# Performance work log

Hardware: AMD Instinct MI355X
Metric: run time of the kernel (lower is better)

The kernel has to match this reference:

```python
import jax, jax.numpy as jnp
import numpy as np

jax.config.update("jax_enable_x64", True)

B, N, M_EQ, D_INEQ = 64, 128, 32, 64
RHO = 1.0
THRES = 1e-5
MAX_ITERS = 5000  # safety cap (original loops until relative objective change <= 1e-5)


def setup_inputs() -> dict:
    key = jax.random.key(0)
    kL, kq, kG, kA, kx0, ks = jax.random.split(key, 6)
    L = jax.random.normal(kL, (B, N, N))
    Q = jnp.einsum('bij,bkj->bik', L, L) / N + jnp.eye(N)  # SPD, well-conditioned
    q = jax.random.normal(kq, (B, N))
    G = jax.random.normal(kG, (B, D_INEQ, N))
    A = jax.random.normal(kA, (B, M_EQ, N))
    x0 = jax.random.normal(kx0, (B, N))
    slack = jax.random.uniform(ks, (B, D_INEQ)) + 0.1
    h = jnp.einsum('bdn,bn->bd', G, x0) + slack  # strictly feasible ineq
    b = jnp.einsum('bmn,bn->bm', A, x0)          # feasible eq
    f32 = jnp.float32
    return {"Q": Q.astype(f32), "q": q.astype(f32), "G": G.astype(f32),
            "h": h.astype(f32), "A": A.astype(f32), "b": b.astype(f32)}


def _alt_diff_batch(Q, q, G, h, A, b):
    """Batched Alt-Diff ADMM QP solve; returns (x [B,n], dx/dq [B,n,n])."""
    Bb, n = q.shape
    d = h.shape[1]
    m = b.shape[1]
    dt = Q.dtype
    AtA = jnp.einsum('bmi,bmj->bij', A, A)
    GtG = jnp.einsum('bdi,bdj->bij', G, G)
    R = -jnp.linalg.inv(Q + RHO * AtA + RHO * GtG)
    ATb = RHO * jnp.einsum('bmn,bm->bn', A, b)
    GTh = RHO * jnp.einsum('bdn,bd->bn', G, h)
    eye = jnp.eye(n, dtype=dt)

    def obj(x):
        return 0.5 * jnp.einsum('bi,bij,bj->b', x, Q, x) + jnp.einsum('bi,bi->b', q, x)

    init = dict(
        xk=jnp.zeros((Bb, n), dt), sk=jnp.zeros((Bb, d), dt),
        lamb=jnp.zeros((Bb, m), dt), nu=jnp.zeros((Bb, d), dt),
        dxk=jnp.zeros((Bb, n, n), dt), dsk=jnp.zeros((Bb, d, n), dt),
        dlamb=jnp.zeros((Bb, m, n), dt), dnu=jnp.zeros((Bb, d, n), dt),
        res_prev=jnp.full((Bb,), 1000.0, dt),   # res = [1000, -100] init
        res_cur=jnp.full((Bb,), -100.0, dt),
        done=jnp.zeros((Bb,), bool),
        it=jnp.zeros((), jnp.int32),
    )

    def cond(s):
        return jnp.logical_and(jnp.any(~s["done"]), s["it"] < MAX_ITERS)

    def body(s):
        xk = jnp.einsum('bij,bj->bi', R,
                        q + jnp.einsum('bmn,bm->bn', A, s["lamb"])
                          + jnp.einsum('bdn,bd->bn', G, s["nu"]) - ATb
                          + RHO * jnp.einsum('bdn,bd->bn', G, s["sk"]) - GTh)
        dxk = jnp.einsum('bij,bjk->bik', R,
                         eye + jnp.einsum('bmn,bmk->bnk', A, s["dlamb"])
                             + jnp.einsum('bdn,bdk->bnk', G, s["dnu"])
                             + RHO * jnp.einsum('bdn,bdk->bnk', G, s["dsk"]))
        Gx = jnp.einsum('bdn,bn->bd', G, xk)
        sk = jax.nn.relu(-(1.0 / RHO) * s["nu"] - (Gx - h))
        sgn = (sk > 0).astype(dt)  # sgn applied to already-relu'd sk, as in source
        dsk = (-1.0 / RHO) * sgn[:, :, None] * (s["dnu"] + RHO * jnp.einsum('bdn,bnk->bdk', G, dxk))
        lamb = s["lamb"] + RHO * (jnp.einsum('bmn,bn->bm', A, xk) - b)
        dlamb = s["dlamb"] + RHO * jnp.einsum('bmn,bnk->bmk', A, dxk)
        nu = s["nu"] + RHO * (Gx + sk - h)
        dnu = s["dnu"] + RHO * (jnp.einsum('bdn,bnk->bdk', G, dxk) + dsk)
        res_new = obj(xk)

        keep = s["done"]

        def sel(old, new):
            mask = keep.reshape((-1,) + (1,) * (new.ndim - 1))
            return jnp.where(mask, old, new)

        res_prev = jnp.where(keep, s["res_prev"], s["res_cur"])
        res_cur = jnp.where(keep, s["res_cur"], res_new)
        done = keep | (jnp.abs((res_cur - res_prev) / res_prev) <= THRES)
        return dict(
            xk=sel(s["xk"], xk), sk=sel(s["sk"], sk),
            lamb=sel(s["lamb"], lamb), nu=sel(s["nu"], nu),
            dxk=sel(s["dxk"], dxk), dsk=sel(s["dsk"], dsk),
            dlamb=sel(s["dlamb"], dlamb), dnu=sel(s["dnu"], dnu),
            res_prev=res_prev, res_cur=res_cur, done=done, it=s["it"] + 1,
        )

    final = jax.lax.while_loop(cond, body, init)
    return final["xk"], final["dxk"]


def reference(Q, q, G, h, A, b):
    out_dtype = q.dtype
    f64 = jnp.float64
    x, _dx = _alt_diff_batch(Q.astype(f64), q.astype(f64), G.astype(f64),
                             h.astype(f64), A.astype(f64), b.astype(f64))
    return x.astype(out_dtype)
```

## Files before the change

### kernel.cpp

```cpp
#include <hip/hip_runtime.h>

#define NN 128
#define ME 32
#define DI 64
#define NZ 96
#define ROWD 130
#define MAXIT 5000

#define OFF_UN 16640
#define ROWB  (OFF_UN)
#define COLB  (OFF_UN + 256)
#define PLO2  (OFF_UN)
#define PHI2  (OFF_UN + 512)
#define TV0   (OFF_UN + 768)
#define TV1   (OFF_UN + 896)
#define FLG   (OFF_UN + 928)
#define YBUF  (OFF_UN)
#define KBUF  (OFF_UN + 1536)
#define CPART (OFF_UN + 1024)
#define VP    (OFF_UN + 1280)
#define BASEV (OFF_UN + 1792)
#define QBV   (OFF_UN + 1888)
#define FPART (OFF_UN + 1024)
#define RHSV  (OFF_UN + 1280)
#define XPART (OFF_UN + 1408)
#define CB    (OFF_UN + 2688)
#define QBUF  (OFF_UN + 2816)
#define V1    (OFF_UN + 2944)
#define V2    (OFF_UN + 3072)
#define HB    (OFF_UN + 3200)
#define BB    (OFF_UN + 3264)
#define CST   (OFF_UN + 3296)
#define ZBF   (OFF_UN + 3304)
#define LDS_DBL (OFF_UN + 3400)

__device__ __forceinline__ float rlf(float v, int lane) {
  return __uint_as_float((unsigned)__builtin_amdgcn_readlane((int)__float_as_uint(v), lane));
}

__global__ __launch_bounds__(256, 1) void altdiff_kernel(
    const float* __restrict__ Qg, const float* __restrict__ qg,
    const float* __restrict__ Gg, const float* __restrict__ hg,
    const float* __restrict__ Ag, const float* __restrict__ bg,
    float* __restrict__ out)
{
  extern __shared__ double ldsd[];
  double2* lds2 = (double2*)ldsd;

  const int bidx = blockIdx.x;
  const int tid  = threadIdx.x;
  const int w    = tid >> 6;
  const int l    = tid & 63;
  const int lm   = l & 31;
  const int ia   = tid & 127;
  const int hh   = tid >> 7;

  const float* Qb = Qg + (size_t)bidx * NN * NN;
  const float* Ab = Ag + (size_t)bidx * ME * NN;
  const float* Gb = Gg + (size_t)bidx * DI * NN;
  const float* qb = qg + (size_t)bidx * NN;
  const float* hb = hg + (size_t)bidx * DI;
  const float* bv = bg + (size_t)bidx * ME;

  if (tid < DI) ldsd[HB + tid] = (double)hb[tid];
  else if (tid < DI + ME) ldsd[BB + tid - DI] = (double)bv[tid - DI];
  if (tid >= 128) ldsd[QBUF + tid - 128] = (double)qb[tid - 128];

  const int r = tid >> 4, c = tid & 15;
  double acc[8][8];

  {
    const float4* Q4 = (const float4*)Qb;
#pragma unroll
    for (int rr = 0; rr < 8; ++rr) {
      float4 q0 = Q4[((8*r+rr) << 5) + 2*c];
      float4 q1 = Q4[((8*r+rr) << 5) + 2*c + 1];
      acc[rr][0]=(double)q0.x; acc[rr][1]=(double)q0.y; acc[rr][2]=(double)q0.z; acc[rr][3]=(double)q0.w;
      acc[rr][4]=(double)q1.x; acc[rr][5]=(double)q1.y; acc[rr][6]=(double)q1.z; acc[rr][7]=(double)q1.w;
    }
    const float4* A4 = (const float4*)Ab;
    for (int m = 0; m < ME; ++m) {
      float4 u0 = A4[(m << 5) + 2*r], u1 = A4[(m << 5) + 2*r + 1];
      float4 v0 = A4[(m << 5) + 2*c], v1 = A4[(m << 5) + 2*c + 1];
      double uu[8] = {(double)u0.x,(double)u0.y,(double)u0.z,(double)u0.w,
                      (double)u1.x,(double)u1.y,(double)u1.z,(double)u1.w};
      double vv[8] = {(double)v0.x,(double)v0.y,(double)v0.z,(double)v0.w,
                      (double)v1.x,(double)v1.y,(double)v1.z,(double)v1.w};
#pragma unroll
      for (int rr = 0; rr < 8; ++rr)
#pragma unroll
        for (int cc = 0; cc < 8; ++cc)
          acc[rr][cc] = fma(uu[rr], vv[cc], acc[rr][cc]);
    }
    const float4* G4 = (const float4*)Gb;
    for (int d = 0; d < DI; ++d) {
      float4 u0 = G4[(d << 5) + 2*r], u1 = G4[(d << 5) + 2*r + 1];
      float4 v0 = G4[(d << 5) + 2*c], v1 = G4[(d << 5) + 2*c + 1];
      double uu[8] = {(double)u0.x,(double)u0.y,(double)u0.z,(double)u0.w,
                      (double)u1.x,(double)u1.y,(double)u1.z,(double)u1.w};
      double vv[8] = {(double)v0.x,(double)v0.y,(double)v0.z,(double)v0.w,
                      (double)v1.x,(double)v1.y,(double)v1.z,(double)v1.w};
#pragma unroll
      for (int rr = 0; rr < 8; ++rr)
#pragma unroll
        for (int cc = 0; cc < 8; ++cc)
          acc[rr][cc] = fma(uu[rr], vv[cc], acc[rr][cc]);
    }
  }

  {
    if (r == 0) {
#pragma unroll
      for (int cc = 0; cc < 8; ++cc) ldsd[ROWB + 8*c + cc] = acc[0][cc];
    }
    if (c == 0) {
#pragma unroll
      for (int rr = 0; rr < 8; ++rr) ldsd[COLB + 8*r + rr] = acc[rr][0];
    }
    __syncthreads();
    for (int k = 0; k < NN; ++k) {
      const int pb = (k & 1) << 7;
      const int krt = k >> 3, kcl = k & 7;
      double rowk[8], colv[8];
#pragma unroll
      for (int cc = 0; cc < 8; ++cc) rowk[cc] = ldsd[ROWB + pb + 8*c + cc];
#pragma unroll
      for (int rr = 0; rr < 8; ++rr) colv[rr] = ldsd[COLB + pb + 8*r + rr];
      const double dkk  = ldsd[ROWB + pb + k];
      const double rcpd = 1.0 / dkk;
      double rdv[8];
#pragma unroll
      for (int cc = 0; cc < 8; ++cc) rdv[cc] = rowk[cc] * rcpd;
      const bool pivR = (r == krt), pivC = (c == krt);
#pragma unroll
      for (int rr = 0; rr < 8; ++rr) {
        const double cv = colv[rr] * rcpd;
        const bool pr = pivR && (rr == kcl);
#pragma unroll
        for (int cc = 0; cc < 8; ++cc) {
          double gen = fma(-cv, rowk[cc], acc[rr][cc]);
          acc[rr][cc] = pr ? rdv[cc] : gen;
        }
      }
      if (pivC) {
#pragma unroll
        for (int cc = 0; cc < 8; ++cc) if (cc == kcl) {
#pragma unroll
          for (int rr = 0; rr < 8; ++rr) {
            const bool pr2 = pivR && (rr == kcl);
            acc[rr][cc] = pr2 ? -rcpd : colv[rr] * rcpd;
          }
        }
      }
      if (k < NN - 1) {
        const int pb2 = ((k + 1) & 1) << 7;
        const int krt2 = (k + 1) >> 3, kcl2 = (k + 1) & 7;
        if (r == krt2) {
#pragma unroll
          for (int rr = 0; rr < 8; ++rr) if (rr == kcl2) {
#pragma unroll
            for (int cc = 0; cc < 8; ++cc) ldsd[ROWB + pb2 + 8*c + cc] = acc[rr][cc];
          }
        }
        if (c == krt2) {
#pragma unroll
          for (int cc = 0; cc < 8; ++cc) if (cc == kcl2) {
#pragma unroll
            for (int rr = 0; rr < 8; ++rr) ldsd[COLB + pb2 + 8*r + rr] = acc[rr][cc];
          }
        }
      }
      __syncthreads();
    }
#pragma unroll
    for (int rr = 0; rr < 8; ++rr) {
      double2* dst = (double2*)(ldsd + (8*r+rr)*ROWD + 8*c);
#pragma unroll
      for (int t = 0; t < 4; ++t) dst[t] = make_double2(acc[rr][2*t], acc[rr][2*t+1]);
    }
  }
  __syncthreads();

  float Kf[24], Kf2[24];
  for (int blk = 0; blk < 8; ++blk) {
    {
      const float* gp[6];
#pragma unroll
      for (int jj = 0; jj < 6; ++jj) {
        int it = 12*blk + 6*hh + jj;
        gp[jj] = (it < DI) ? (Gb + it*NN) : (Ab + (it - DI)*NN);
      }
      double a2[6] = {0,0,0,0,0,0};
#pragma unroll 4
      for (int t = 0; t < NN; ++t) {
        double rv = ldsd[t*ROWD + ia];
#pragma unroll
        for (int jj = 0; jj < 6; ++jj)
          a2[jj] = fma(rv, (double)gp[jj][t], a2[jj]);
      }
      double2* yst = (double2*)(ldsd + YBUF + ia*12 + 6*hh);
#pragma unroll
      for (int p = 0; p < 3; ++p) yst[p] = make_double2(a2[2*p], a2[2*p+1]);
    }
    __syncthreads();
    {
      const int r2 = (ia < NZ) ? ia : 0;
      const float* brow = (r2 < DI) ? (Gb + r2*NN) : (Ab + (r2 - DI)*NN);
      double a2[6] = {0,0,0,0,0,0};
#pragma unroll 4
      for (int t = 0; t < NN; ++t) {
        double bvv = (double)brow[t];
        const double2* yr = (const double2*)(ldsd + YBUF + t*12 + 6*hh);
        double2 y0 = yr[0], y1 = yr[1], y2 = yr[2];
        a2[0] = fma(bvv, y0.x, a2[0]); a2[1] = fma(bvv, y0.y, a2[1]);
        a2[2] = fma(bvv, y1.x, a2[2]); a2[3] = fma(bvv, y1.y, a2[3]);
        a2[4] = fma(bvv, y2.x, a2[4]); a2[5] = fma(bvv, y2.y, a2[5]);
      }
      if (ia < NZ) {
#pragma unroll
        for (int jj = 0; jj < 6; ++jj) ldsd[KBUF + (6*hh + jj)*NZ + ia] = a2[jj];
      }
    }
    __syncthreads();
    if (w == (blk >> 1)) {
      if ((blk & 1) == 0) {
#pragma unroll
        for (int jj = 0; jj < 12; ++jj) {
          Kf [jj] = (float)ldsd[KBUF + jj*NZ + l];
          Kf2[jj] = (float)ldsd[KBUF + jj*NZ + 64 + lm];
        }
      } else {
#pragma unroll
        for (int jj = 0; jj < 12; ++jj) {
          Kf [12+jj] = (float)ldsd[KBUF + jj*NZ + l];
          Kf2[12+jj] = (float)ldsd[KBUF + jj*NZ + 64 + lm];
        }
      }
    }
    __syncthreads();
  }

  {
    double s = 0;
#pragma unroll 8
    for (int jc = 0; jc < 48; ++jc) {
      int j = 48*hh + jc;
      double coef = (j < DI) ? ldsd[HB + j] : ldsd[BB + j - DI];
      const float* src = (j < DI) ? (Gb + j*NN) : (Ab + (j - DI)*NN);
      s = fma(-(double)src[ia], coef, s);
    }
    ldsd[CPART + hh*128 + ia] = s;
  }
  __syncthreads();
  if (tid < NN) ldsd[CB + tid] = ldsd[QBUF + tid] + ldsd[CPART + tid] + ldsd[CPART + 128 + tid];
  __syncthreads();

  {
    double a = 0, b2 = 0;
#pragma unroll 4
    for (int tt = 0; tt < 64; ++tt) {
      int t = 64*hh + tt;
      double rv = ldsd[t*ROWD + ia];
      a  = fma(rv, ldsd[CB + t], a);
      b2 = fma(rv, ldsd[QBUF + t], b2);
    }
    ldsd[VP + hh*128 + ia] = a;
    ldsd[VP + 256 + hh*128 + ia] = b2;
  }
  __syncthreads();
  if (tid < NN) {
    ldsd[V1 + tid] = ldsd[VP + tid] + ldsd[VP + 128 + tid];
    ldsd[V2 + tid] = ldsd[VP + 256 + tid] + ldsd[VP + 384 + tid];
  }
  __syncthreads();

  {
    const int r2 = (ia < NZ) ? ia : 0;
    const float* brow = (r2 < DI) ? (Gb + r2*NN) : (Ab + (r2 - DI)*NN);
    const int voff = hh ? V2 : V1;
    double s = 0;
#pragma unroll 4
    for (int t = 0; t < NN; ++t) s = fma((double)brow[t], ldsd[voff + t], s);
    if (ia < NZ) ldsd[(hh ? QBV : BASEV) + ia] = s;
  }
  if (w == 0) {
    double pc = ldsd[V1+l]*ldsd[CB+l]   + ldsd[V1+64+l]*ldsd[CB+64+l];
    double pq = ldsd[V1+l]*ldsd[QBUF+l] + ldsd[V1+64+l]*ldsd[QBUF+64+l];
#pragma unroll
    for (int off = 32; off >= 1; off >>= 1) { pc += __shfl_xor(pc, off); pq += __shfl_xor(pq, off); }
    if (l == 0) { ldsd[CST] = pc; ldsd[CST+1] = pq; }
  }
  __syncthreads();

  const double h_r   = ldsd[HB + l];
  const double b_r   = ldsd[BB + lm];
  const double baseA = ldsd[BASEV + l];
  const double baseB = ldsd[BASEV + 64 + lm];
  const double qvA   = ldsd[QBV + l];
  const double qvB   = ldsd[QBV + 64 + lm];
  const double S_uc  = ldsd[CST], S_qu = ldsd[CST + 1];
  double nu = 0.0, lam = 0.0;
  double zlo = 0.0, zhi = 0.0;
  double zAlo = 0.0, zAhi = 0.0, zBlo = 0.0, zBhi = 0.0, zClo = 0.0, zChi = 0.0;
  double res_prev = 1000.0, res_cur = -100.0;

  {
    double a0 = (w == 0) ? baseA : 0.0;
    double a1 = (w == 0) ? baseB : 0.0;
    ldsd[PLO2 + w*64 + l] = a0;
    if (l < 32) ldsd[PHI2 + w*32 + l] = a1;
    if (tid == 0) { ldsd[FLG] = 0.0; ldsd[FLG + 1] = 0.0; }
  }

  for (int it = 0; it < MAXIT + 3; ++it) {
    __syncthreads();
    const int p  = (it & 1) << 8;
    const int ph = (it & 1) << 7;
    const int bprev = (it + 1) & 1;
    double fl = ldsd[FLG + bprev];
    double t1v[16];
    if (w == 1) {
      const double2* tp = (const double2*)(ldsd + TV1 + bprev*16);
#pragma unroll
      for (int u = 0; u < 8; ++u) { double2 v = tp[u]; t1v[2*u] = v.x; t1v[2*u+1] = v.y; }
    }
    double a40 = 0, a41 = 0, a42 = 0, a43 = 0;
    if (w == 3) {
      const double2* t0p = (const double2*)(ldsd + TV0 + bprev*64 + (l & 15)*4);
      double2 v0 = t0p[0], v1 = t0p[1];
      a40 = v0.x; a41 = v0.y; a42 = v1.x; a43 = v1.y;
    }
    double ylo = 0.0, yhi = 0.0;
    if (w != 3)
      ylo = (ldsd[PLO2 + p + l]       + ldsd[PLO2 + p + 64 + l])
          + (ldsd[PLO2 + p + 128 + l] + ldsd[PLO2 + p + 192 + l]);
    if (w >= 2)
      yhi = (ldsd[PHI2 + ph + lm]      + ldsd[PHI2 + ph + 32 + lm])
          + (ldsd[PHI2 + ph + 64 + lm] + ldsd[PHI2 + ph + 96 + lm]);
    if (it >= 3 && fl != 0.0) break;
    if (w == 2) { zClo = zBlo; zChi = zBhi; zBlo = zAlo; zBhi = zAhi; zAlo = zlo; zAhi = zhi; }
    if (it < MAXIT) {
      if (w != 3) {
        double sk = fmax(0.0, -nu - ylo + h_r);
        nu  = nu + ylo + sk - h_r;
        zlo = nu + sk;
      }
      if (w >= 2) {
        lam = lam + yhi - b_r;
        zhi = lam;
      }
      const float zflo = (float)zlo;
      const float zfhi = (float)zhi;
      float a0f = 0.f, a0g = 0.f, a1f = 0.f, a1g = 0.f;
      if (w == 0) {
#pragma unroll
        for (int j = 0; j < 24; j += 2) {
          float zj  = rlf(zflo, j);
          float zj1 = rlf(zflo, j + 1);
          a0f = fmaf(Kf[j],   zj,  a0f); a1f = fmaf(Kf2[j],   zj,  a1f);
          a0g = fmaf(Kf[j+1], zj1, a0g); a1g = fmaf(Kf2[j+1], zj1, a1g);
        }
      } else if (w == 1) {
#pragma unroll
        for (int j = 0; j < 24; j += 2) {
          float zj  = rlf(zflo, 24 + j);
          float zj1 = rlf(zflo, 24 + j + 1);
          a0f = fmaf(Kf[j],   zj,  a0f); a1f = fmaf(Kf2[j],   zj,  a1f);
          a0g = fmaf(Kf[j+1], zj1, a0g); a1g = fmaf(Kf2[j+1], zj1, a1g);
        }
      } else if (w == 2) {
#pragma unroll
        for (int j = 0; j < 16; j += 2) {
          float zj  = rlf(zflo, 48 + j);
          float zj1 = rlf(zflo, 48 + j + 1);
          a0f = fmaf(Kf[j],   zj,  a0f); a1f = fmaf(Kf2[j],   zj,  a1f);
          a0g = fmaf(Kf[j+1], zj1, a0g); a1g = fmaf(Kf2[j+1], zj1, a1g);
        }
#pragma unroll
        for (int j = 0; j < 8; j += 2) {
          float zj  = rlf(zfhi, j);
          float zj1 = rlf(zfhi, j + 1);
          a0f = fmaf(Kf[16+j],   zj,  a0f); a1f = fmaf(Kf2[16+j],   zj,  a1f);
          a0g = fmaf(Kf[16+j+1], zj1, a0g); a1g = fmaf(Kf2[16+j+1], zj1, a1g);
        }
      } else {
#pragma unroll
        for (int j = 0; j < 24; j += 2) {
          float zj  = rlf(zfhi, 8 + j);
          float zj1 = rlf(zfhi, 8 + j + 1);
          a0f = fmaf(Kf[j],   zj,  a0f); a1f = fmaf(Kf2[j],   zj,  a1f);
          a0g = fmaf(Kf[j+1], zj1, a0g); a1g = fmaf(Kf2[j+1], zj1, a1g);
        }
      }
      double pa0 = (double)(a0f + a0g);
      double pa1 = (double)(a1f + a1g);
      if (w == 0) { pa0 += baseA; pa1 += baseB; }
      ldsd[PLO2 + (p ^ 256) + w*64 + l] = pa0;
      if (l < 32) ldsd[PHI2 + (ph ^ 128) + w*32 + l] = pa1;
      if (w == 2) {
        double tv = fma(qvA, zAlo, -0.5*(zAlo*(baseA + ylo) + ylo*ylo));
        tv += (l < 32) ? fma(qvB, zAhi, -0.5*(zAhi*(baseB + yhi) + yhi*yhi)) : 0.0;
        ldsd[TV0 + (it & 1)*64 + l] = tv;
      }
    }
    if (w == 3 && l < 16 && it >= 1 && it <= MAXIT)
      ldsd[TV1 + (it & 1)*16 + l] = (a40 + a41) + (a42 + a43);
    if (w == 1 && it >= 2 && it <= MAXIT + 1) {
      double s1 = ((t1v[0] + t1v[1]) + (t1v[2] + t1v[3])) + ((t1v[4] + t1v[5]) + (t1v[6] + t1v[7]));
      double s2 = ((t1v[8] + t1v[9]) + (t1v[10] + t1v[11])) + ((t1v[12] + t1v[13]) + (t1v[14] + t1v[15]));
      double obj = (s1 + s2) - 0.5*S_uc + S_qu;
      res_prev = res_cur; res_cur = obj;
      if (l == 0)
        ldsd[FLG + (it & 1)] = (fabs((res_cur - res_prev) / res_prev) <= 1e-5) ? 1.0 : 0.0;
    }
  }

  if (w == 2) {
    ldsd[ZBF + l] = zClo;
    if (l < 32) ldsd[ZBF + 64 + l] = zChi;
  }
  __syncthreads();
  {
    double s = 0;
#pragma unroll 8
    for (int jc = 0; jc < 48; ++jc) {
      int j = 48*hh + jc;
      double zj = ldsd[ZBF + j];
      const float* src = (j < DI) ? (Gb + j*NN) : (Ab + (j - DI)*NN);
      s = fma((double)src[ia], zj, s);
    }
    ldsd[FPART + hh*128 + ia] = s;
  }
  __syncthreads();
  if (tid < NN) ldsd[RHSV + tid] = ldsd[CB + tid] + ldsd[FPART + tid] + ldsd[FPART + 128 + tid];
  __syncthreads();
  {
    double s = 0;
#pragma unroll 4
    for (int tt = 0; tt < 64; ++tt) {
      int t = 64*hh + tt;
      s = fma(ldsd[t*ROWD + ia], ldsd[RHSV + t], s);
    }
    ldsd[XPART + hh*128 + ia] = s;
  }
  __syncthreads();
  if (tid < NN)
    out[(size_t)bidx * NN + tid] = (float)(ldsd[XPART + tid] + ldsd[XPART + 128 + tid]);
}

extern "C" void kernel_launch(void* const* d_in, const int* in_sizes, int n_in,
                              void* d_out, int out_size, void* d_ws, size_t ws_size,
                              hipStream_t stream) {
  (void)in_sizes; (void)n_in; (void)out_size; (void)d_ws; (void)ws_size;
  const float* Q = (const float*)d_in[0];
  const float* q = (const float*)d_in[1];
  const float* G = (const float*)d_in[2];
  const float* h = (const float*)d_in[3];
  const float* A = (const float*)d_in[4];
  const float* b = (const float*)d_in[5];
  float* out = (float*)d_out;
  const size_t lds_bytes = (size_t)LDS_DBL * sizeof(double);
  altdiff_kernel<<<dim3(64), dim3(256), lds_bytes, stream>>>(Q, q, G, h, A, b, out);
}
```

Baseline: 656.5 us.

## Pack per-wave partial sums as interleaved floats and use packed FMA in ADMM loop

The per-iteration partial products across the four waves are now stored as fp32, interleaved four per element with an XOR swizzle, so each lane reads them back with one float4 load instead of four separate double loads. The matvec uses two-wide float vectors so the compiler can emit packed FMA instructions. The baseA/baseB addition moves to the reader, the nu/sk update is simplified algebraically, and the convergence test replaces the division with a multiply. Partial sums are now stored and reduced in float rather than double, which slightly changes the rounding of y.

```diff
diff --git a/kernel.cpp b/kernel.cpp
--- a/kernel.cpp
+++ b/kernel.cpp
@@ -10,11 +10,11 @@
 #define OFF_UN 16640
 #define ROWB  (OFF_UN)
 #define COLB  (OFF_UN + 256)
-#define PLO2  (OFF_UN)
-#define PHI2  (OFF_UN + 512)
-#define TV0   (OFF_UN + 768)
-#define TV1   (OFF_UN + 896)
-#define FLG   (OFF_UN + 928)
+#define FPLO  (2*OFF_UN)
+#define FPHI  (2*OFF_UN + 512)
+#define TV0   (OFF_UN + 384)
+#define TV1   (OFF_UN + 512)
+#define FLG   (OFF_UN + 544)
 #define YBUF  (OFF_UN)
 #define KBUF  (OFF_UN + 1536)
 #define CPART (OFF_UN + 1024)
@@ -34,8 +34,13 @@
 #define ZBF   (OFF_UN + 3304)
 #define LDS_DBL (OFF_UN + 3400)
 
+typedef __attribute__((ext_vector_type(2))) float f32x2;
+
 __device__ __forceinline__ float rlf(float v, int lane) {
   return __uint_as_float((unsigned)__builtin_amdgcn_readlane((int)__float_as_uint(v), lane));
+}
+__device__ __forceinline__ f32x2 fma2(f32x2 a, f32x2 b, f32x2 c) {
+  return __builtin_elementwise_fma(a, b, c);
 }
 
 __global__ __launch_bounds__(256, 1) void altdiff_kernel(
@@ -45,7 +50,7 @@
     float* __restrict__ out)
 {
   extern __shared__ double ldsd[];
-  double2* lds2 = (double2*)ldsd;
+  float* const ldsf = (float*)ldsd;
 
   const int bidx = blockIdx.x;
   const int tid  = threadIdx.x;
@@ -181,7 +186,7 @@
   }
   __syncthreads();
 
-  float Kf[24], Kf2[24];
+  f32x2 Kp[12], Kp2[12];
   for (int blk = 0; blk < 8; ++blk) {
     {
       const float* gp[6];
@@ -225,15 +230,19 @@
     if (w == (blk >> 1)) {
       if ((blk & 1) == 0) {
 #pragma unroll
-        for (int jj = 0; jj < 12; ++jj) {
-          Kf [jj] = (float)ldsd[KBUF + jj*NZ + l];
-          Kf2[jj] = (float)ldsd[KBUF + jj*NZ + 64 + lm];
+        for (int p = 0; p < 6; ++p) {
+          Kp [p].x = (float)ldsd[KBUF + (2*p  )*NZ + l];
+          Kp [p].y = (float)ldsd[KBUF + (2*p+1)*NZ + l];
+          Kp2[p].x = (float)ldsd[KBUF + (2*p  )*NZ + 64 + lm];
+          Kp2[p].y = (float)ldsd[KBUF + (2*p+1)*NZ + 64 + lm];
         }
       } else {
 #pragma unroll
-        for (int jj = 0; jj < 12; ++jj) {
-          Kf [12+jj] = (float)ldsd[KBUF + jj*NZ + l];
-          Kf2[12+jj] = (float)ldsd[KBUF + jj*NZ + 64 + lm];
+        for (int p = 0; p < 6; ++p) {
+          Kp [6+p].x = (float)ldsd[KBUF + (2*p  )*NZ + l];
+          Kp [6+p].y = (float)ldsd[KBUF + (2*p+1)*NZ + l];
+          Kp2[6+p].x = (float)ldsd[KBUF + (2*p  )*NZ + 64 + lm];
+          Kp2[6+p].y = (float)ldsd[KBUF + (2*p+1)*NZ + 64 + lm];
         }
       }
     }
@@ -305,19 +314,20 @@
   double res_prev = 1000.0, res_cur = -100.0;
 
   {
-    double a0 = (w == 0) ? baseA : 0.0;
-    double a1 = (w == 0) ? baseB : 0.0;
-    ldsd[PLO2 + w*64 + l] = a0;
-    if (l < 32) ldsd[PHI2 + w*32 + l] = a1;
+    ldsf[FPLO + 4*l + (w ^ (l & 3))] = 0.f;
+    if (l < 32) ldsf[FPHI + 4*lm + (w ^ (lm & 3))] = 0.f;
     if (tid == 0) { ldsd[FLG] = 0.0; ldsd[FLG + 1] = 0.0; }
   }
 
   for (int it = 0; it < MAXIT + 3; ++it) {
     __syncthreads();
-    const int p  = (it & 1) << 8;
-    const int ph = (it & 1) << 7;
+    const int pf  = (it & 1) << 8;
+    const int phf = (it & 1) << 7;
     const int bprev = (it + 1) & 1;
     double fl = ldsd[FLG + bprev];
+    float4 plo = {0.f, 0.f, 0.f, 0.f}, phi4 = {0.f, 0.f, 0.f, 0.f};
+    if (w != 3) plo  = *(const float4*)&ldsf[FPLO + pf  + 4*l];
+    if (w >= 2) phi4 = *(const float4*)&ldsf[FPHI + phf + 4*lm];
     double t1v[16];
     if (w == 1) {
       const double2* tp = (const double2*)(ldsd + TV1 + bprev*16);
@@ -326,82 +336,80 @@
     }
     double a40 = 0, a41 = 0, a42 = 0, a43 = 0;
     if (w == 3) {
-      const double2* t0p = (const double2*)(ldsd + TV0 + bprev*64 + (l & 15)*4);
-      double2 v0 = t0p[0], v1 = t0p[1];
-      a40 = v0.x; a41 = v0.y; a42 = v1.x; a43 = v1.y;
+      const int g = l & 15;
+      const double* tb = ldsd + TV0 + bprev*64;
+      a40 = tb[g]; a41 = tb[g + 16]; a42 = tb[g + 32]; a43 = tb[g + 48];
     }
     double ylo = 0.0, yhi = 0.0;
-    if (w != 3)
-      ylo = (ldsd[PLO2 + p + l]       + ldsd[PLO2 + p + 64 + l])
-          + (ldsd[PLO2 + p + 128 + l] + ldsd[PLO2 + p + 192 + l]);
-    if (w >= 2)
-      yhi = (ldsd[PHI2 + ph + lm]      + ldsd[PHI2 + ph + 32 + lm])
-          + (ldsd[PHI2 + ph + 64 + lm] + ldsd[PHI2 + ph + 96 + lm]);
+    if (w != 3) ylo = (double)((plo.x + plo.y) + (plo.z + plo.w)) + baseA;
+    if (w >= 2) yhi = (double)((phi4.x + phi4.y) + (phi4.z + phi4.w)) + baseB;
     if (it >= 3 && fl != 0.0) break;
     if (w == 2) { zClo = zBlo; zChi = zBhi; zBlo = zAlo; zBhi = zAhi; zAlo = zlo; zAhi = zhi; }
     if (it < MAXIT) {
+      float zflo = 0.f, zfhi = 0.f;
       if (w != 3) {
-        double sk = fmax(0.0, -nu - ylo + h_r);
-        nu  = nu + ylo + sk - h_r;
+        double t  = (h_r - nu) - ylo;
+        double sk = fmax(t, 0.0);
+        nu  = sk - t;
         zlo = nu + sk;
+        zflo = (float)zlo;
       }
       if (w >= 2) {
         lam = lam + yhi - b_r;
         zhi = lam;
-      }
-      const float zflo = (float)zlo;
-      const float zfhi = (float)zhi;
-      float a0f = 0.f, a0g = 0.f, a1f = 0.f, a1g = 0.f;
-      if (w == 0) {
-#pragma unroll
-        for (int j = 0; j < 24; j += 2) {
-          float zj  = rlf(zflo, j);
-          float zj1 = rlf(zflo, j + 1);
-          a0f = fmaf(Kf[j],   zj,  a0f); a1f = fmaf(Kf2[j],   zj,  a1f);
-          a0g = fmaf(Kf[j+1], zj1, a0g); a1g = fmaf(Kf2[j+1], zj1, a1g);
-        }
-      } else if (w == 1) {
-#pragma unroll
-        for (int j = 0; j < 24; j += 2) {
-          float zj  = rlf(zflo, 24 + j);
-          float zj1 = rlf(zflo, 24 + j + 1);
-          a0f = fmaf(Kf[j],   zj,  a0f); a1f = fmaf(Kf2[j],   zj,  a1f);
-          a0g = fmaf(Kf[j+1], zj1, a0g); a1g = fmaf(Kf2[j+1], zj1, a1g);
-        }
-      } else if (w == 2) {
-#pragma unroll
-        for (int j = 0; j < 16; j += 2) {
-          float zj  = rlf(zflo, 48 + j);
-          float zj1 = rlf(zflo, 48 + j + 1);
-          a0f = fmaf(Kf[j],   zj,  a0f); a1f = fmaf(Kf2[j],   zj,  a1f);
-          a0g = fmaf(Kf[j+1], zj1, a0g); a1g = fmaf(Kf2[j+1], zj1, a1g);
-        }
-#pragma unroll
-        for (int j = 0; j < 8; j += 2) {
-          float zj  = rlf(zfhi, j);
-          float zj1 = rlf(zfhi, j + 1);
-          a0f = fmaf(Kf[16+j],   zj,  a0f); a1f = fmaf(Kf2[16+j],   zj,  a1f);
-          a0g = fmaf(Kf[16+j+1], zj1, a0g); a1g = fmaf(Kf2[16+j+1], zj1, a1g);
-        }
-      } else {
-#pragma unroll
-        for (int j = 0; j < 24; j += 2) {
-          float zj  = rlf(zfhi, 8 + j);
-          float zj1 = rlf(zfhi, 8 + j + 1);
-          a0f = fmaf(Kf[j],   zj,  a0f); a1f = fmaf(Kf2[j],   zj,  a1f);
-          a0g = fmaf(Kf[j+1], zj1, a0g); a1g = fmaf(Kf2[j+1], zj1, a1g);
-        }
-      }
-      double pa0 = (double)(a0f + a0g);
-      double pa1 = (double)(a1f + a1g);
-      if (w == 0) { pa0 += baseA; pa1 += baseB; }
-      ldsd[PLO2 + (p ^ 256) + w*64 + l] = pa0;
-      if (l < 32) ldsd[PHI2 + (ph ^ 128) + w*32 + l] = pa1;
+        zfhi = (float)zhi;
+      }
       if (w == 2) {
         double tv = fma(qvA, zAlo, -0.5*(zAlo*(baseA + ylo) + ylo*ylo));
         tv += (l < 32) ? fma(qvB, zAhi, -0.5*(zAhi*(baseB + yhi) + yhi*yhi)) : 0.0;
         ldsd[TV0 + (it & 1)*64 + l] = tv;
       }
+      f32x2 A0 = {0.f, 0.f}, A1 = A0, B0 = A0, B1 = A0;
+      if (w == 0) {
+#pragma unroll
+        for (int p = 0; p < 12; p += 2) {
+          f32x2 z0 = {rlf(zflo, 2*p),     rlf(zflo, 2*p + 1)};
+          A0 = fma2(Kp[p],   z0, A0); B0 = fma2(Kp2[p],   z0, B0);
+          f32x2 z1 = {rlf(zflo, 2*p + 2), rlf(zflo, 2*p + 3)};
+          A1 = fma2(Kp[p+1], z1, A1); B1 = fma2(Kp2[p+1], z1, B1);
+        }
+      } else if (w == 1) {
+#pragma unroll
+        for (int p = 0; p < 12; p += 2) {
+          f32x2 z0 = {rlf(zflo, 24 + 2*p),     rlf(zflo, 24 + 2*p + 1)};
+          A0 = fma2(Kp[p],   z0, A0); B0 = fma2(Kp2[p],   z0, B0);
+          f32x2 z1 = {rlf(zflo, 24 + 2*p + 2), rlf(zflo, 24 + 2*p + 3)};
+          A1 = fma2(Kp[p+1], z1, A1); B1 = fma2(Kp2[p+1], z1, B1);
+        }
+      } else if (w == 2) {
+#pragma unroll
+        for (int p = 0; p < 8; p += 2) {
+          f32x2 z0 = {rlf(zflo, 48 + 2*p),     rlf(zflo, 48 + 2*p + 1)};
+          A0 = fma2(Kp[p],   z0, A0); B0 = fma2(Kp2[p],   z0, B0);
+          f32x2 z1 = {rlf(zflo, 48 + 2*p + 2), rlf(zflo, 48 + 2*p + 3)};
+          A1 = fma2(Kp[p+1], z1, A1); B1 = fma2(Kp2[p+1], z1, B1);
+        }
+#pragma unroll
+        for (int p = 8; p < 12; p += 2) {
+          f32x2 z0 = {rlf(zfhi, 2*(p-8)),     rlf(zfhi, 2*(p-8) + 1)};
+          A0 = fma2(Kp[p],   z0, A0); B0 = fma2(Kp2[p],   z0, B0);
+          f32x2 z1 = {rlf(zfhi, 2*(p-7)),     rlf(zfhi, 2*(p-7) + 1)};
+          A1 = fma2(Kp[p+1], z1, A1); B1 = fma2(Kp2[p+1], z1, B1);
+        }
+      } else {
+#pragma unroll
+        for (int p = 0; p < 12; p += 2) {
+          f32x2 z0 = {rlf(zfhi, 8 + 2*p),     rlf(zfhi, 8 + 2*p + 1)};
+          A0 = fma2(Kp[p],   z0, A0); B0 = fma2(Kp2[p],   z0, B0);
+          f32x2 z1 = {rlf(zfhi, 8 + 2*p + 2), rlf(zfhi, 8 + 2*p + 3)};
+          A1 = fma2(Kp[p+1], z1, A1); B1 = fma2(Kp2[p+1], z1, B1);
+        }
+      }
+      f32x2 As = A0 + A1, Bs = B0 + B1;
+      float pa0 = As.x + As.y;
+      float pa1 = Bs.x + Bs.y;
+      ldsf[FPLO + (pf ^ 256) + 4*l + (w ^ (l & 3))] = pa0;
+      if (l < 32) ldsf[FPHI + (phf ^ 128) + 4*lm + (w ^ (lm & 3))] = pa1;
     }
     if (w == 3 && l < 16 && it >= 1 && it <= MAXIT)
       ldsd[TV1 + (it & 1)*16 + l] = (a40 + a41) + (a42 + a43);
@@ -411,7 +419,7 @@
       double obj = (s1 + s2) - 0.5*S_uc + S_qu;
       res_prev = res_cur; res_cur = obj;
       if (l == 0)
-        ldsd[FLG + (it & 1)] = (fabs((res_cur - res_prev) / res_prev) <= 1e-5) ? 1.0 : 0.0;
+        ldsd[FLG + (it & 1)] = (fabs(res_cur - res_prev) <= 1e-5 * fabs(res_prev)) ? 1.0 : 0.0;
     }
   }
 
```

Result: no change. 661.0 us (+0.7%).
